# Optimization experiments

Measured on AMD Instinct MI355X. Metric: run time of the kernel, lower is better.

The kernel has to match this reference:

```python
import jax, jax.numpy as jnp
import numpy as np

# ---- static config (mirrors build() with the chosen init_kwargs) ----
B, H, W, C = 16, 56, 56, 128
KH, KW = 3, 3          # filter_size
SH, SW = 1, 1          # stride
NF = 256               # n_filters
IN_FEAT = C * KH * KW  # 1152
NNZ = int(1 * 0.2 * IN_FEAT * NF)  # multiple * density * n_parameters = 58982


def _make_indices():
    """Replicates the full='output' sparsity-pattern construction from build()."""
    rng = np.random.default_rng(0)
    per_col = NNZ // NF
    remain = NNZ % NF
    remain_cols = set(rng.choice(NF, remain, replace=False).tolist())
    chunks = []
    for col in rng.permutation(NF):
        k = per_col + (1 if int(col) in remain_cols else 0)
        rows = rng.choice(IN_FEAT, k, replace=False)
        chunks.append(np.stack([rows, np.full(k, col, dtype=np.int64)], axis=1))
    return np.concatenate(chunks, axis=0).astype(np.int32)  # (NNZ, 2) [row, col]


def setup_inputs() -> dict:
    key = jax.random.key(0)
    k1, k2 = jax.random.split(key)
    x = jax.random.normal(k1, (B, H, W, C), dtype=jnp.float32)
    limit = float(np.sqrt(6.0 / (IN_FEAT + NF)))  # glorot_uniform on the sparse values
    kernel = jax.random.uniform(k2, (NNZ,), jnp.float32, -limit, limit)
    bias = jnp.zeros((NF,), jnp.float32)
    indices = jnp.asarray(_make_indices())
    return {"x": x, "kernel": kernel, "bias": bias, "indices": indices}


def _im2col_valid(x):
    # tf.image.extract_patches ordering: patch positions row-major (di, dj),
    # channels fastest -> concatenate C-channel slices in (di, dj) order.
    oh = (H - KH) // SH + 1
    ow = (W - KW) // SW + 1
    cols = [x[:, di:di + oh * SH:SH, dj:dj + ow * SW:SW, :]
            for di in range(KH) for dj in range(KW)]
    return jnp.concatenate(cols, axis=-1), oh, ow  # (B, oh, ow, IN_FEAT)


def reference(x, kernel, bias, indices):
    patches, oh, ow = _im2col_valid(x)
    pm = patches.reshape(-1, IN_FEAT)  # (B*oh*ow, IN_FEAT)
    # Sparse (IN_FEAT, NF) weight: scatter values into a dense matrix
    # (indices are unique by construction, so .add == .set and is grad-safe).
    Wm = jnp.zeros((IN_FEAT, NF), dtype=pm.dtype).at[indices[:, 0], indices[:, 1]].add(kernel)
    out = pm @ Wm + bias            # sparse-dense matmul + bias
    out = jax.nn.relu(out)          # activation
    return out.reshape(B, oh, ow, NF)
```

## Files before the change

kernel.cpp:

```cpp
#include <hip/hip_runtime.h>

typedef unsigned short u16;
typedef __bf16 bf16x8 __attribute__((ext_vector_type(8)));
typedef float f32x4 __attribute__((ext_vector_type(4)));

#define B_   16
#define H_   56
#define W_   56
#define C_   128
#define OH_  54
#define OW_  54
#define NF_  256
#define KF_  1152
#define M_   46656
#define NNZ_ 58982

#define XB_ELEMS (B_*H_*W_*C_)
#define WT_ELEMS (36*4*256*8)

__device__ __forceinline__ u16 f2bf(float f) {
    unsigned u = __float_as_uint(f);
    u += 0x7FFFu + ((u >> 16) & 1u);
    return (u16)(u >> 16);
}

__device__ __forceinline__ void gload16(const void* g, void* l) {
    __builtin_amdgcn_global_load_lds(
        (const __attribute__((address_space(1))) unsigned int*)g,
        (__attribute__((address_space(3))) unsigned int*)l,
        16, 0, 0);
}

__global__ __launch_bounds__(256) void cvt_x_kernel(const float* __restrict__ x,
                                                    u16* __restrict__ xb,
                                                    u16* __restrict__ wt) {
    if (blockIdx.x < 144) {
        uint4 z = {0u, 0u, 0u, 0u};
        ((uint4*)wt)[blockIdx.x * 256 + threadIdx.x] = z;
    }
    int i = (blockIdx.x * 256 + threadIdx.x) * 8;
    float4 v0 = *(const float4*)(x + i);
    float4 v1 = *(const float4*)(x + i + 4);
    union { u16 u[8]; uint4 v; } r;
    r.u[0] = f2bf(v0.x); r.u[1] = f2bf(v0.y); r.u[2] = f2bf(v0.z); r.u[3] = f2bf(v0.w);
    r.u[4] = f2bf(v1.x); r.u[5] = f2bf(v1.y); r.u[6] = f2bf(v1.z); r.u[7] = f2bf(v1.w);
    *(uint4*)(xb + i) = r.v;
}

__global__ __launch_bounds__(256) void scatter_kernel(const float* __restrict__ kv,
                                                      const int* __restrict__ idx,
                                                      u16* __restrict__ wt) {
    int t = blockIdx.x * 256 + threadIdx.x;
    if (t >= NNZ_) return;
    int k   = idx[2*t];
    int col = idx[2*t + 1];
    int kt = k >> 5, ks = (k >> 3) & 3, e = k & 7;
    wt[(kt * 4 + ks) * 2048 + col * 8 + e] = f2bf(kv[t]);
}

__global__ __launch_bounds__(256) void spconv_gemm(const u16* __restrict__ xb,
                                                   const u16* __restrict__ wt,
                                                   const float* __restrict__ bias,
                                                   float* __restrict__ out) {
    __shared__ __align__(16) u16 As[2][64 * 32];
    __shared__ __align__(16) u16 Bs[2][4 * 128 * 8];

    const int t    = threadIdx.x;
    const int lane = t & 63;
    const int wid  = t >> 6;

    const int nwg = gridDim.x;
    const int q = nwg >> 3, r = nwg & 7;
    const int xcd = blockIdx.x & 7, inner = blockIdx.x >> 3;
    const int wg = (xcd < r ? xcd * (q + 1) : r * (q + 1) + (xcd - r) * q) + inner;
    const int mi = wg >> 1;
    const int ni = wg & 1;
    const int m0 = mi * 64;

    const int arow = t >> 2;
    const int kc   = t & 3;
    const int kcs  = kc ^ (arow & 3) ^ ((arow >> 2) & 3);
    const int kco  = kcs * 8;
    int mg  = m0 + arow;
    int bb  = mg / (OH_ * OW_);
    int rem = mg % (OH_ * OW_);
    int ii  = rem / OW_;
    int jj  = rem % OW_;
    const u16* a_base = xb + ((bb * H_ + ii) * W_ + jj) * C_;
    const int a_dst = t * 8;

    const u16* b_src0 = wt + (t >> 7) * 2048 + ni * 1024 + (t & 127) * 8;
    const u16* b_src1 = b_src0 + 2 * 2048;
    const int b_dst0 = t * 8;
    const int b_dst1 = t * 8 + 2048;

    f32x4 acc[2][4];
    const f32x4 zz = {0.f, 0.f, 0.f, 0.f};
#pragma unroll
    for (int i = 0; i < 2; ++i)
#pragma unroll
        for (int j = 0; j < 4; ++j) acc[i][j] = zz;

    const int ks  = lane >> 4;
    const int r16 = lane & 15;
    const int cidx = ks ^ (r16 & 3) ^ ((r16 >> 2) & 3);
    const int wr = wid >> 1;
    const int wc = wid & 1;

#define ISSUE(kn, bi) do {                                                  \
    int g_  = (kn) >> 2;                                                    \
    int di_ = (g_ * 11) >> 5;                                               \
    int dj_ = g_ - 3 * di_;                                                 \
    int aoff_ = (di_ * W_ + dj_) * C_ + ((kn) & 3) * 32 + kco;              \
    gload16(a_base + aoff_, &As[bi][0] + a_dst);                            \
    gload16(b_src0 + (kn) * 8192, &Bs[bi][0] + b_dst0);                     \
    gload16(b_src1 + (kn) * 8192, &Bs[bi][0] + b_dst1);                     \
} while (0)

#define COMPUTE(bi) do {                                                    \
    bf16x8 a0_ = *(const bf16x8*)(&As[bi][(wr * 32 + r16) * 32 + cidx * 8]);\
    bf16x8 a1_ = *(const bf16x8*)(&As[bi][(wr * 32 + 16 + r16) * 32 + cidx * 8]); \
    _Pragma("unroll")                                                       \
    for (int nf = 0; nf < 4; ++nf) {                                        \
        bf16x8 b_ = *(const bf16x8*)(&Bs[bi][(ks * 128 + wc * 64 + nf * 16 + r16) * 8]); \
        acc[0][nf] = __builtin_amdgcn_mfma_f32_16x16x32_bf16(a0_, b_, acc[0][nf], 0, 0, 0); \
        acc[1][nf] = __builtin_amdgcn_mfma_f32_16x16x32_bf16(a1_, b_, acc[1][nf], 0, 0, 0); \
    }                                                                       \
} while (0)

#define WAITVM(n) asm volatile("s_waitcnt vmcnt(" #n ")" ::: "memory")
#define BAR() do { __builtin_amdgcn_s_barrier();                            \
                   asm volatile("" ::: "memory"); } while (0)

    ISSUE(0, 0);
    ISSUE(1, 1);

#pragma unroll
    for (int k = 0; k < 34; ++k) {
        WAITVM(3);
        BAR();
        COMPUTE(k & 1);
        BAR();
        ISSUE(k + 2, k & 1);
    }
    WAITVM(3); BAR(); COMPUTE(0); BAR();
    WAITVM(0); BAR(); COMPUTE(1);

#undef ISSUE
#undef COMPUTE
#undef WAITVM
#undef BAR

    const int rgrp = lane >> 4;
#pragma unroll
    for (int nf = 0; nf < 4; ++nf) {
        int col  = ni * 128 + wc * 64 + nf * 16 + r16;
        float bv = bias[col];
#pragma unroll
        for (int mf = 0; mf < 2; ++mf) {
#pragma unroll
            for (int rr = 0; rr < 4; ++rr) {
                int row = m0 + wr * 32 + mf * 16 + rgrp * 4 + rr;
                float v = acc[mf][nf][rr] + bv;
                out[row * NF_ + col] = fmaxf(v, 0.f);
            }
        }
    }
}

extern "C" void kernel_launch(void* const* d_in, const int* in_sizes, int n_in,
                              void* d_out, int out_size, void* d_ws, size_t ws_size,
                              hipStream_t stream) {
    const float* x    = (const float*)d_in[0];
    const float* kv   = (const float*)d_in[1];
    const float* bias = (const float*)d_in[2];
    const int*   idx  = (const int*)d_in[3];
    float* out = (float*)d_out;

    u16* xb  = (u16*)d_ws;
    u16* wtp = (u16*)((char*)d_ws + (size_t)XB_ELEMS * 2);

    cvt_x_kernel<<<XB_ELEMS / (256 * 8), 256, 0, stream>>>(x, xb, wtp);
    scatter_kernel<<<(NNZ_ + 255) / 256, 256, 0, stream>>>(kv, idx, wtp);
    spconv_gemm<<<(M_ / 64) * 2, 256, 0, stream>>>(xb, wtp, bias, out);
}
```

Measured before the change: 49.73 us.

## Restructure GEMM to 64x256 tiles with 32x32 MFMA and register-resident B

Each workgroup now computes a full 64x256 output tile with two waves (128 threads) instead of two 64x128 tiles across four waves. This halves redundant im2col A loads. It switches to 32x32x16 bf16 MFMA and loads the weight fragments straight from global into registers with inline global_load_dwordx4, dropping the B shared-memory staging. The cost is much higher register pressure (large accumulators plus double-buffered B fragments) and fewer waves per CU.

```diff
diff --git a/kernel.cpp b/kernel.cpp
--- a/kernel.cpp
+++ b/kernel.cpp
@@ -2,7 +2,7 @@
 
 typedef unsigned short u16;
 typedef __bf16 bf16x8 __attribute__((ext_vector_type(8)));
-typedef float f32x4 __attribute__((ext_vector_type(4)));
+typedef float f32x16 __attribute__((ext_vector_type(16)));
 
 #define B_   16
 #define H_   56
@@ -58,111 +58,140 @@
     wt[(kt * 4 + ks) * 2048 + col * 8 + e] = f2bf(kv[t]);
 }
 
-__global__ __launch_bounds__(256) void spconv_gemm(const u16* __restrict__ xb,
-                                                   const u16* __restrict__ wt,
-                                                   const float* __restrict__ bias,
-                                                   float* __restrict__ out) {
+__global__ __launch_bounds__(128, 2) void spconv_gemm(const u16* __restrict__ xb,
+                                                      const u16* __restrict__ wt,
+                                                      const float* __restrict__ bias,
+                                                      float* __restrict__ out) {
     __shared__ __align__(16) u16 As[2][64 * 32];
-    __shared__ __align__(16) u16 Bs[2][4 * 128 * 8];
-
-    const int t    = threadIdx.x;
-    const int lane = t & 63;
-    const int wid  = t >> 6;
+
+    const int t   = threadIdx.x;
+    const int l   = t & 63;
+    const int w   = t >> 6;
+    const int l31 = l & 31;
+    const int hi  = l >> 5;
 
     const int nwg = gridDim.x;
     const int q = nwg >> 3, r = nwg & 7;
     const int xcd = blockIdx.x & 7, inner = blockIdx.x >> 3;
     const int wg = (xcd < r ? xcd * (q + 1) : r * (q + 1) + (xcd - r) * q) + inner;
-    const int mi = wg >> 1;
-    const int ni = wg & 1;
-    const int m0 = mi * 64;
-
-    const int arow = t >> 2;
-    const int kc   = t & 3;
-    const int kcs  = kc ^ (arow & 3) ^ ((arow >> 2) & 3);
-    const int kco  = kcs * 8;
-    int mg  = m0 + arow;
-    int bb  = mg / (OH_ * OW_);
-    int rem = mg % (OH_ * OW_);
-    int ii  = rem / OW_;
-    int jj  = rem % OW_;
-    const u16* a_base = xb + ((bb * H_ + ii) * W_ + jj) * C_;
-    const int a_dst = t * 8;
-
-    const u16* b_src0 = wt + (t >> 7) * 2048 + ni * 1024 + (t & 127) * 8;
-    const u16* b_src1 = b_src0 + 2 * 2048;
-    const int b_dst0 = t * 8;
-    const int b_dst1 = t * 8 + 2048;
-
-    f32x4 acc[2][4];
-    const f32x4 zz = {0.f, 0.f, 0.f, 0.f};
+    const int m0 = wg * 64;
+
+    const int row0 = t >> 2;
+    const int kco  = ((t & 3) ^ ((t >> 2) & 3)) * 8;
+    const u16* a_base0;
+    const u16* a_base1;
+    {
+#define MKBASE(dst, mg) do {                                   \
+        int bb_  = (mg) / (OH_ * OW_);                         \
+        int rem_ = (mg) % (OH_ * OW_);                         \
+        int ii_  = rem_ / OW_;                                 \
+        int jj_  = rem_ % OW_;                                 \
+        dst = xb + ((bb_ * H_ + ii_) * W_ + jj_) * C_;         \
+    } while (0)
+        MKBASE(a_base0, m0 + row0);
+        MKBASE(a_base1, m0 + row0 + 32);
+#undef MKBASE
+    }
+
+    const char* wtb = (const char*)wt;
+    const char* b0 = wtb + hi * 4096 + w * 2048 + l31 * 16;
+    const char* b1 = b0 + 8192;
+
+    int aoffr[2][2];
+#pragma unroll
+    for (int rb = 0; rb < 2; ++rb)
+#pragma unroll
+        for (int kp = 0; kp < 2; ++kp)
+            aoffr[rb][kp] = ((rb * 32 + l31) * 4 + ((kp * 2 + hi) ^ (l & 3))) * 8;
+
+    f32x16 acc[2][4];
 #pragma unroll
     for (int i = 0; i < 2; ++i)
 #pragma unroll
-        for (int j = 0; j < 4; ++j) acc[i][j] = zz;
-
-    const int ks  = lane >> 4;
-    const int r16 = lane & 15;
-    const int cidx = ks ^ (r16 & 3) ^ ((r16 >> 2) & 3);
-    const int wr = wid >> 1;
-    const int wc = wid & 1;
-
-#define ISSUE(kn, bi) do {                                                  \
+        for (int j = 0; j < 4; ++j) acc[i][j] = (f32x16)0.f;
+
+    bf16x8 bS0[8], bS1[8];
+
+#define LOADB(dst, base, imm) \
+    asm volatile("global_load_dwordx4 %0, %1, off offset:" imm \
+                 : "=v"(dst) : "v"(base) : "memory")
+
+#define ISSUE_A(kn, bi) do {                                                \
     int g_  = (kn) >> 2;                                                    \
     int di_ = (g_ * 11) >> 5;                                               \
     int dj_ = g_ - 3 * di_;                                                 \
     int aoff_ = (di_ * W_ + dj_) * C_ + ((kn) & 3) * 32 + kco;              \
-    gload16(a_base + aoff_, &As[bi][0] + a_dst);                            \
-    gload16(b_src0 + (kn) * 8192, &Bs[bi][0] + b_dst0);                     \
-    gload16(b_src1 + (kn) * 8192, &Bs[bi][0] + b_dst1);                     \
+    gload16(a_base0 + aoff_, &As[bi][t * 8]);                               \
+    gload16(a_base1 + aoff_, &As[bi][(t + 128) * 8]);                       \
 } while (0)
 
-#define COMPUTE(bi) do {                                                    \
-    bf16x8 a0_ = *(const bf16x8*)(&As[bi][(wr * 32 + r16) * 32 + cidx * 8]);\
-    bf16x8 a1_ = *(const bf16x8*)(&As[bi][(wr * 32 + 16 + r16) * 32 + cidx * 8]); \
+#define ISSUE_B(bset) do {                                                  \
+    LOADB(bset[0], b0, "0");    LOADB(bset[1], b0, "512");                  \
+    LOADB(bset[2], b0, "1024"); LOADB(bset[3], b0, "1536");                 \
+    LOADB(bset[4], b1, "0");    LOADB(bset[5], b1, "512");                  \
+    LOADB(bset[6], b1, "1024"); LOADB(bset[7], b1, "1536");                 \
+    b0 += 16384; b1 += 16384;                                               \
+} while (0)
+
+#define COMPUTE(bi, bset) do {                                              \
+    bf16x8 af_[2][2];                                                       \
     _Pragma("unroll")                                                       \
-    for (int nf = 0; nf < 4; ++nf) {                                        \
-        bf16x8 b_ = *(const bf16x8*)(&Bs[bi][(ks * 128 + wc * 64 + nf * 16 + r16) * 8]); \
-        acc[0][nf] = __builtin_amdgcn_mfma_f32_16x16x32_bf16(a0_, b_, acc[0][nf], 0, 0, 0); \
-        acc[1][nf] = __builtin_amdgcn_mfma_f32_16x16x32_bf16(a1_, b_, acc[1][nf], 0, 0, 0); \
-    }                                                                       \
+    for (int rb = 0; rb < 2; ++rb)                                          \
+        _Pragma("unroll")                                                   \
+        for (int kp = 0; kp < 2; ++kp)                                      \
+            af_[rb][kp] = *(const bf16x8*)(&As[bi][aoffr[rb][kp]]);         \
+    _Pragma("unroll")                                                       \
+    for (int kp = 0; kp < 2; ++kp)                                          \
+        _Pragma("unroll")                                                   \
+        for (int rb = 0; rb < 2; ++rb)                                      \
+            _Pragma("unroll")                                               \
+            for (int cb = 0; cb < 4; ++cb)                                  \
+                acc[rb][cb] = __builtin_amdgcn_mfma_f32_32x32x16_bf16(      \
+                    af_[rb][kp], bset[kp * 4 + cb], acc[rb][cb], 0, 0, 0);  \
 } while (0)
 
 #define WAITVM(n) asm volatile("s_waitcnt vmcnt(" #n ")" ::: "memory")
+#define WAITLG0() asm volatile("s_waitcnt lgkmcnt(0)" ::: "memory")
+#define SB0()     __builtin_amdgcn_sched_barrier(0)
 #define BAR() do { __builtin_amdgcn_s_barrier();                            \
                    asm volatile("" ::: "memory"); } while (0)
 
-    ISSUE(0, 0);
-    ISSUE(1, 1);
-
-#pragma unroll
-    for (int k = 0; k < 34; ++k) {
-        WAITVM(3);
-        BAR();
-        COMPUTE(k & 1);
-        BAR();
-        ISSUE(k + 2, k & 1);
-    }
-    WAITVM(3); BAR(); COMPUTE(0); BAR();
-    WAITVM(0); BAR(); COMPUTE(1);
-
-#undef ISSUE
+    ISSUE_A(0, 0); ISSUE_B(bS0);
+    ISSUE_A(1, 1); ISSUE_B(bS1);
+
+    for (int k2 = 0; k2 < 17; ++k2) {
+        int kn0 = 2 * k2 + 2, kn1 = 2 * k2 + 3;
+        WAITVM(10); SB0(); BAR();
+        COMPUTE(0, bS0);
+        WAITLG0(); BAR();
+        ISSUE_A(kn0, 0); ISSUE_B(bS0);
+        WAITVM(10); SB0(); BAR();
+        COMPUTE(1, bS1);
+        WAITLG0(); BAR();
+        ISSUE_A(kn1, 1); ISSUE_B(bS1);
+    }
+    WAITVM(10); SB0(); BAR(); COMPUTE(0, bS0);
+    WAITVM(0);  SB0(); BAR(); COMPUTE(1, bS1);
+
+#undef LOADB
+#undef ISSUE_A
+#undef ISSUE_B
 #undef COMPUTE
 #undef WAITVM
+#undef WAITLG0
+#undef SB0
 #undef BAR
 
-    const int rgrp = lane >> 4;
-#pragma unroll
-    for (int nf = 0; nf < 4; ++nf) {
-        int col  = ni * 128 + wc * 64 + nf * 16 + r16;
+#pragma unroll
+    for (int cb = 0; cb < 4; ++cb) {
+        int col  = w * 128 + cb * 32 + l31;
         float bv = bias[col];
 #pragma unroll
-        for (int mf = 0; mf < 2; ++mf) {
-#pragma unroll
-            for (int rr = 0; rr < 4; ++rr) {
-                int row = m0 + wr * 32 + mf * 16 + rgrp * 4 + rr;
-                float v = acc[mf][nf][rr] + bv;
-                out[row * NF_ + col] = fmaxf(v, 0.f);
+        for (int rb = 0; rb < 2; ++rb) {
+#pragma unroll
+            for (int rg = 0; rg < 16; ++rg) {
+                int row = m0 + rb * 32 + (rg & 3) + 8 * (rg >> 2) + 4 * hi;
+                out[row * NF_ + col] = fmaxf(acc[rb][cb][rg] + bv, 0.f);
             }
         }
     }
@@ -182,5 +211,5 @@
 
     cvt_x_kernel<<<XB_ELEMS / (256 * 8), 256, 0, stream>>>(x, xb, wtp);
     scatter_kernel<<<(NNZ_ + 255) / 256, 256, 0, stream>>>(kv, idx, wtp);
-    spconv_gemm<<<(M_ / 64) * 2, 256, 0, stream>>>(xb, wtp, bias, out);
-}
+    spconv_gemm<<<M_ / 64, 128, 0, stream>>>(xb, wtp, bias, out);
+}
```

After: 45.66 us. 8.2% less time.

## Widen GEMM tile to all 256 columns, load B directly to registers

Applied to the files above, without the earlier changes.

Each workgroup now computes a 64x256 output tile instead of 64x128, with each wave owning 64 columns, so the A im2col tile is loaded once per row block instead of twice. B fragments are read straight from global memory into registers with inline asm loads, dropping the B shared-memory staging. A uses a triple-buffered LDS ring with a deeper prefetch and adjusted vmcnt waits. Register pressure rises (16 accumulators plus three B register sets), and launch bounds request 3 blocks per SM. The grid is also halved.

```diff
diff --git a/kernel.cpp b/kernel.cpp
--- a/kernel.cpp
+++ b/kernel.cpp
@@ -58,12 +58,11 @@
     wt[(kt * 4 + ks) * 2048 + col * 8 + e] = f2bf(kv[t]);
 }
 
-__global__ __launch_bounds__(256) void spconv_gemm(const u16* __restrict__ xb,
-                                                   const u16* __restrict__ wt,
-                                                   const float* __restrict__ bias,
-                                                   float* __restrict__ out) {
-    __shared__ __align__(16) u16 As[2][64 * 32];
-    __shared__ __align__(16) u16 Bs[2][4 * 128 * 8];
+__global__ __launch_bounds__(256, 3) void spconv_gemm(const u16* __restrict__ xb,
+                                                      const u16* __restrict__ wt,
+                                                      const float* __restrict__ bias,
+                                                      float* __restrict__ out) {
+    __shared__ __align__(16) u16 As[3][64 * 32];
 
     const int t    = threadIdx.x;
     const int lane = t & 63;
@@ -73,58 +72,64 @@
     const int q = nwg >> 3, r = nwg & 7;
     const int xcd = blockIdx.x & 7, inner = blockIdx.x >> 3;
     const int wg = (xcd < r ? xcd * (q + 1) : r * (q + 1) + (xcd - r) * q) + inner;
-    const int mi = wg >> 1;
-    const int ni = wg & 1;
-    const int m0 = mi * 64;
+    const int m0 = wg * 64;
 
     const int arow = t >> 2;
-    const int kc   = t & 3;
-    const int kcs  = kc ^ (arow & 3) ^ ((arow >> 2) & 3);
-    const int kco  = kcs * 8;
-    int mg  = m0 + arow;
-    int bb  = mg / (OH_ * OW_);
-    int rem = mg % (OH_ * OW_);
-    int ii  = rem / OW_;
-    int jj  = rem % OW_;
-    const u16* a_base = xb + ((bb * H_ + ii) * W_ + jj) * C_;
-    const int a_dst = t * 8;
-
-    const u16* b_src0 = wt + (t >> 7) * 2048 + ni * 1024 + (t & 127) * 8;
-    const u16* b_src1 = b_src0 + 2 * 2048;
-    const int b_dst0 = t * 8;
-    const int b_dst1 = t * 8 + 2048;
-
-    f32x4 acc[2][4];
+    const int kco  = ((t & 3) ^ (arow & 3) ^ ((arow >> 2) & 3)) * 8;
+    const u16* a_base;
+    {
+        int mg  = m0 + arow;
+        int bb  = mg / (OH_ * OW_);
+        int rem = mg % (OH_ * OW_);
+        int ii  = rem / OW_;
+        int jj  = rem % OW_;
+        a_base = xb + ((bb * H_ + ii) * W_ + jj) * C_;
+    }
+
+    const int ks   = lane >> 4;
+    const int r16  = lane & 15;
+    const int cidx = ks ^ (r16 & 3) ^ ((r16 >> 2) & 3);
+
+    const char* bptr = (const char*)wt + ks * 4096 + (wid * 64 + r16) * 16;
+
+    f32x4 acc[4][4];
     const f32x4 zz = {0.f, 0.f, 0.f, 0.f};
 #pragma unroll
-    for (int i = 0; i < 2; ++i)
+    for (int i = 0; i < 4; ++i)
 #pragma unroll
         for (int j = 0; j < 4; ++j) acc[i][j] = zz;
 
-    const int ks  = lane >> 4;
-    const int r16 = lane & 15;
-    const int cidx = ks ^ (r16 & 3) ^ ((r16 >> 2) & 3);
-    const int wr = wid >> 1;
-    const int wc = wid & 1;
-
-#define ISSUE(kn, bi) do {                                                  \
+    bf16x8 bs[3][4];
+
+#define LOADB(dst, base, imm) \
+    asm volatile("global_load_dwordx4 %0, %1, off offset:" imm \
+                 : "=v"(dst) : "v"(base))
+
+#define ISSUE_B(si) do {                                                    \
+    LOADB(bs[si][0], bptr, "0");   LOADB(bs[si][1], bptr, "256");           \
+    LOADB(bs[si][2], bptr, "512"); LOADB(bs[si][3], bptr, "768");           \
+    bptr += 16384;                                                          \
+} while (0)
+
+#define ISSUE_A(kn, bi) do {                                                \
     int g_  = (kn) >> 2;                                                    \
     int di_ = (g_ * 11) >> 5;                                               \
     int dj_ = g_ - 3 * di_;                                                 \
     int aoff_ = (di_ * W_ + dj_) * C_ + ((kn) & 3) * 32 + kco;              \
-    gload16(a_base + aoff_, &As[bi][0] + a_dst);                            \
-    gload16(b_src0 + (kn) * 8192, &Bs[bi][0] + b_dst0);                     \
-    gload16(b_src1 + (kn) * 8192, &Bs[bi][0] + b_dst1);                     \
+    gload16(a_base + aoff_, &As[bi][t * 8]);                                \
 } while (0)
 
-#define COMPUTE(bi) do {                                                    \
-    bf16x8 a0_ = *(const bf16x8*)(&As[bi][(wr * 32 + r16) * 32 + cidx * 8]);\
-    bf16x8 a1_ = *(const bf16x8*)(&As[bi][(wr * 32 + 16 + r16) * 32 + cidx * 8]); \
+#define COMPUTE(bi, si) do {                                                \
+    bf16x8 a0_ = *(const bf16x8*)(&As[bi][(r16) * 32 + cidx * 8]);          \
+    bf16x8 a1_ = *(const bf16x8*)(&As[bi][(16 + r16) * 32 + cidx * 8]);     \
+    bf16x8 a2_ = *(const bf16x8*)(&As[bi][(32 + r16) * 32 + cidx * 8]);     \
+    bf16x8 a3_ = *(const bf16x8*)(&As[bi][(48 + r16) * 32 + cidx * 8]);     \
     _Pragma("unroll")                                                       \
     for (int nf = 0; nf < 4; ++nf) {                                        \
-        bf16x8 b_ = *(const bf16x8*)(&Bs[bi][(ks * 128 + wc * 64 + nf * 16 + r16) * 8]); \
-        acc[0][nf] = __builtin_amdgcn_mfma_f32_16x16x32_bf16(a0_, b_, acc[0][nf], 0, 0, 0); \
-        acc[1][nf] = __builtin_amdgcn_mfma_f32_16x16x32_bf16(a1_, b_, acc[1][nf], 0, 0, 0); \
+        acc[0][nf] = __builtin_amdgcn_mfma_f32_16x16x32_bf16(a0_, bs[si][nf], acc[0][nf], 0, 0, 0); \
+        acc[1][nf] = __builtin_amdgcn_mfma_f32_16x16x32_bf16(a1_, bs[si][nf], acc[1][nf], 0, 0, 0); \
+        acc[2][nf] = __builtin_amdgcn_mfma_f32_16x16x32_bf16(a2_, bs[si][nf], acc[2][nf], 0, 0, 0); \
+        acc[3][nf] = __builtin_amdgcn_mfma_f32_16x16x32_bf16(a3_, bs[si][nf], acc[3][nf], 0, 0, 0); \
     }                                                                       \
 } while (0)
 
@@ -132,21 +137,32 @@
 #define BAR() do { __builtin_amdgcn_s_barrier();                            \
                    asm volatile("" ::: "memory"); } while (0)
 
-    ISSUE(0, 0);
-    ISSUE(1, 1);
-
-#pragma unroll
-    for (int k = 0; k < 34; ++k) {
-        WAITVM(3);
+    ISSUE_B(0);
+    ISSUE_A(0, 0);
+    ISSUE_B(1);
+    ISSUE_A(1, 1);
+    ISSUE_A(2, 2);
+
+#pragma unroll
+    for (int k = 0; k < 33; ++k) {
+        WAITVM(6); BAR();
+        ISSUE_B((k + 2) % 3);
+        COMPUTE(k % 3, k % 3);
         BAR();
-        COMPUTE(k & 1);
-        BAR();
-        ISSUE(k + 2, k & 1);
-    }
-    WAITVM(3); BAR(); COMPUTE(0); BAR();
-    WAITVM(0); BAR(); COMPUTE(1);
-
-#undef ISSUE
+        ISSUE_A(k + 3, k % 3);
+    }
+    WAITVM(6); BAR();
+    ISSUE_B(2);
+    COMPUTE(0, 0);
+    BAR();
+    WAITVM(5); BAR();
+    COMPUTE(1, 1);
+    WAITVM(0); BAR();
+    COMPUTE(2, 2);
+
+#undef LOADB
+#undef ISSUE_B
+#undef ISSUE_A
 #undef COMPUTE
 #undef WAITVM
 #undef BAR
@@ -154,13 +170,13 @@
     const int rgrp = lane >> 4;
 #pragma unroll
     for (int nf = 0; nf < 4; ++nf) {
-        int col  = ni * 128 + wc * 64 + nf * 16 + r16;
+        int col  = wid * 64 + nf * 16 + r16;
         float bv = bias[col];
 #pragma unroll
-        for (int mf = 0; mf < 2; ++mf) {
+        for (int mf = 0; mf < 4; ++mf) {
 #pragma unroll
             for (int rr = 0; rr < 4; ++rr) {
-                int row = m0 + wr * 32 + mf * 16 + rgrp * 4 + rr;
+                int row = m0 + mf * 16 + rgrp * 4 + rr;
                 float v = acc[mf][nf][rr] + bv;
                 out[row * NF_ + col] = fmaxf(v, 0.f);
             }
@@ -182,5 +198,5 @@
 
     cvt_x_kernel<<<XB_ELEMS / (256 * 8), 256, 0, stream>>>(x, xb, wtp);
     scatter_kernel<<<(NNZ_ + 255) / 256, 256, 0, stream>>>(kv, idx, wtp);
-    spconv_gemm<<<(M_ / 64) * 2, 256, 0, stream>>>(xb, wtp, bias, out);
-}
+    spconv_gemm<<<M_ / 64, 256, 0, stream>>>(xb, wtp, bias, out);
+}
```

After: 42.63 us. 1.17x faster.

## Enlarge GEMM tile to 192x256 with 512 threads and 64-wide K steps

Applied to the files above, without the earlier changes.

The implicit-GEMM kernel now gives each 512-thread block a 192-row tile covering all 256 output columns, instead of a 64x128 tile per 256-thread block. Each K step is 64 wide instead of 32. The packed weight layout and the LDS swizzle are changed to match. The goal is to stop reloading each A tile for both N halves and to raise MFMA work per LDS and global load, which should cut memory traffic and barrier overhead. In exchange, LDS use (112KB) and accumulator registers go up, the grid drops to 243 blocks with at most one block per CU, and the XCD-aware block remapping is removed.

```diff
diff --git a/kernel.cpp b/kernel.cpp
--- a/kernel.cpp
+++ b/kernel.cpp
@@ -16,7 +16,7 @@
 #define NNZ_ 58982
 
 #define XB_ELEMS (B_*H_*W_*C_)
-#define WT_ELEMS (36*4*256*8)
+#define WT_ELEMS (KF_*NF_)
 
 __device__ __forceinline__ u16 f2bf(float f) {
     unsigned u = __float_as_uint(f);
@@ -54,77 +54,77 @@
     if (t >= NNZ_) return;
     int k   = idx[2*t];
     int col = idx[2*t + 1];
-    int kt = k >> 5, ks = (k >> 3) & 3, e = k & 7;
-    wt[(kt * 4 + ks) * 2048 + col * 8 + e] = f2bf(kv[t]);
+    wt[(k >> 3) * 2048 + col * 8 + (k & 7)] = f2bf(kv[t]);
 }
 
-__global__ __launch_bounds__(256) void spconv_gemm(const u16* __restrict__ xb,
-                                                   const u16* __restrict__ wt,
-                                                   const float* __restrict__ bias,
-                                                   float* __restrict__ out) {
-    __shared__ __align__(16) u16 As[2][64 * 32];
-    __shared__ __align__(16) u16 Bs[2][4 * 128 * 8];
+__global__ __launch_bounds__(512, 2) void spconv_gemm(const u16* __restrict__ xb,
+                                                      const u16* __restrict__ wt,
+                                                      const float* __restrict__ bias,
+                                                      float* __restrict__ out) {
+    __shared__ __align__(16) u16 As[2][12288];
+    __shared__ __align__(16) u16 Bs[2][16384];
 
     const int t    = threadIdx.x;
-    const int lane = t & 63;
-    const int wid  = t >> 6;
+    const int l    = t & 63;
+    const int w    = t >> 6;
+    const int r16  = l & 15;
+    const int ks   = l >> 4;
+    const int wr   = w >> 2;
+    const int wc   = w & 3;
+    const int m0   = blockIdx.x * 192;
 
-    const int nwg = gridDim.x;
-    const int q = nwg >> 3, r = nwg & 7;
-    const int xcd = blockIdx.x & 7, inner = blockIdx.x >> 3;
-    const int wg = (xcd < r ? xcd * (q + 1) : r * (q + 1) + (xcd - r) * q) + inner;
-    const int mi = wg >> 1;
-    const int ni = wg & 1;
-    const int m0 = mi * 64;
+    const int r0  = t >> 3;
+    const int sd  = t & 7;
+    const int kco = (sd ^ (r0 & 7)) * 8;
+    const u16* a_base[3];
+#pragma unroll
+    for (int j = 0; j < 3; ++j) {
+        int mg  = m0 + r0 + j * 64;
+        int bb  = mg / (OH_ * OW_);
+        int rem = mg % (OH_ * OW_);
+        int ii  = rem / OW_;
+        int jj  = rem % OW_;
+        a_base[j] = xb + ((bb * H_ + ii) * W_ + jj) * C_;
+    }
 
-    const int arow = t >> 2;
-    const int kc   = t & 3;
-    const int kcs  = kc ^ (arow & 3) ^ ((arow >> 2) & 3);
-    const int kco  = kcs * 8;
-    int mg  = m0 + arow;
-    int bb  = mg / (OH_ * OW_);
-    int rem = mg % (OH_ * OW_);
-    int ii  = rem / OW_;
-    int jj  = rem % OW_;
-    const u16* a_base = xb + ((bb * H_ + ii) * W_ + jj) * C_;
-    const int a_dst = t * 8;
-
-    const u16* b_src0 = wt + (t >> 7) * 2048 + ni * 1024 + (t & 127) * 8;
-    const u16* b_src1 = b_src0 + 2 * 2048;
-    const int b_dst0 = t * 8;
-    const int b_dst1 = t * 8 + 2048;
-
-    f32x4 acc[2][4];
+    f32x4 acc[6][4];
     const f32x4 zz = {0.f, 0.f, 0.f, 0.f};
 #pragma unroll
-    for (int i = 0; i < 2; ++i)
+    for (int i = 0; i < 6; ++i)
 #pragma unroll
         for (int j = 0; j < 4; ++j) acc[i][j] = zz;
 
-    const int ks  = lane >> 4;
-    const int r16 = lane & 15;
-    const int cidx = ks ^ (r16 & 3) ^ ((r16 >> 2) & 3);
-    const int wr = wid >> 1;
-    const int wc = wid & 1;
-
-#define ISSUE(kn, bi) do {                                                  \
-    int g_  = (kn) >> 2;                                                    \
+#define ISSUE(kt, bi) do {                                                  \
+    int g_  = (kt) >> 1;                                                    \
     int di_ = (g_ * 11) >> 5;                                               \
     int dj_ = g_ - 3 * di_;                                                 \
-    int aoff_ = (di_ * W_ + dj_) * C_ + ((kn) & 3) * 32 + kco;              \
-    gload16(a_base + aoff_, &As[bi][0] + a_dst);                            \
-    gload16(b_src0 + (kn) * 8192, &Bs[bi][0] + b_dst0);                     \
-    gload16(b_src1 + (kn) * 8192, &Bs[bi][0] + b_dst1);                     \
+    int apix_ = (di_ * W_ + dj_) * C_ + ((kt) & 1) * 64 + kco;              \
+    gload16(a_base[0] + apix_, &As[bi][t * 8]);                             \
+    gload16(a_base[1] + apix_, &As[bi][t * 8 + 4096]);                      \
+    gload16(a_base[2] + apix_, &As[bi][t * 8 + 8192]);                      \
+    const u16* bsrc_ = wt + (kt) * 16384 + t * 8;                           \
+    gload16(bsrc_,         &Bs[bi][t * 8]);                                 \
+    gload16(bsrc_ + 4096,  &Bs[bi][t * 8 + 4096]);                          \
+    gload16(bsrc_ + 8192,  &Bs[bi][t * 8 + 8192]);                          \
+    gload16(bsrc_ + 12288, &Bs[bi][t * 8 + 12288]);                         \
 } while (0)
 
 #define COMPUTE(bi) do {                                                    \
-    bf16x8 a0_ = *(const bf16x8*)(&As[bi][(wr * 32 + r16) * 32 + cidx * 8]);\
-    bf16x8 a1_ = *(const bf16x8*)(&As[bi][(wr * 32 + 16 + r16) * 32 + cidx * 8]); \
     _Pragma("unroll")                                                       \
-    for (int nf = 0; nf < 4; ++nf) {                                        \
-        bf16x8 b_ = *(const bf16x8*)(&Bs[bi][(ks * 128 + wc * 64 + nf * 16 + r16) * 8]); \
-        acc[0][nf] = __builtin_amdgcn_mfma_f32_16x16x32_bf16(a0_, b_, acc[0][nf], 0, 0, 0); \
-        acc[1][nf] = __builtin_amdgcn_mfma_f32_16x16x32_bf16(a1_, b_, acc[1][nf], 0, 0, 0); \
+    for (int h = 0; h < 2; ++h) {                                           \
+        const int chs_ = ((h * 4 + ks) ^ (r16 & 7)) * 8;                    \
+        bf16x8 af_[6];                                                      \
+        _Pragma("unroll")                                                   \
+        for (int mf = 0; mf < 6; ++mf)                                      \
+            af_[mf] = *(const bf16x8*)(&As[bi][(wr * 96 + mf * 16 + r16) * 64 + chs_]); \
+        _Pragma("unroll")                                                   \
+        for (int nf = 0; nf < 4; ++nf) {                                    \
+            bf16x8 bf_ = *(const bf16x8*)(&Bs[bi][((h * 4 + ks) * 256 + wc * 64 + nf * 16 + r16) * 8]); \
+            _Pragma("unroll")                                               \
+            for (int mf = 0; mf < 6; ++mf)                                  \
+                acc[mf][nf] = __builtin_amdgcn_mfma_f32_16x16x32_bf16(      \
+                    af_[mf], bf_, acc[mf][nf], 0, 0, 0);                    \
+        }                                                                   \
     }                                                                       \
 } while (0)
 
@@ -136,14 +136,14 @@
     ISSUE(1, 1);
 
 #pragma unroll
-    for (int k = 0; k < 34; ++k) {
-        WAITVM(3);
+    for (int k = 0; k < 16; ++k) {
+        WAITVM(7);
         BAR();
         COMPUTE(k & 1);
         BAR();
         ISSUE(k + 2, k & 1);
     }
-    WAITVM(3); BAR(); COMPUTE(0); BAR();
+    WAITVM(7); BAR(); COMPUTE(0);
     WAITVM(0); BAR(); COMPUTE(1);
 
 #undef ISSUE
@@ -151,16 +151,15 @@
 #undef WAITVM
 #undef BAR
 
-    const int rgrp = lane >> 4;
 #pragma unroll
     for (int nf = 0; nf < 4; ++nf) {
-        int col  = ni * 128 + wc * 64 + nf * 16 + r16;
+        int col  = wc * 64 + nf * 16 + r16;
         float bv = bias[col];
 #pragma unroll
-        for (int mf = 0; mf < 2; ++mf) {
+        for (int mf = 0; mf < 6; ++mf) {
 #pragma unroll
             for (int rr = 0; rr < 4; ++rr) {
-                int row = m0 + wr * 32 + mf * 16 + rgrp * 4 + rr;
+                int row = m0 + wr * 96 + mf * 16 + ks * 4 + rr;
                 float v = acc[mf][nf][rr] + bv;
                 out[row * NF_ + col] = fmaxf(v, 0.f);
             }
@@ -182,5 +181,5 @@
 
     cvt_x_kernel<<<XB_ELEMS / (256 * 8), 256, 0, stream>>>(x, xb, wtp);
     scatter_kernel<<<(NNZ_ + 255) / 256, 256, 0, stream>>>(kv, idx, wtp);
-    spconv_gemm<<<(M_ / 64) * 2, 256, 0, stream>>>(xb, wtp, bias, out);
+    spconv_gemm<<<M_ / 192, 512, 0, stream>>>(xb, wtp, bias, out);
 }
```

Result: no change. 50.32 us (+1.2%).
